# Optimization experiments

Measured on AMD Instinct MI355X. Metric: run time of the kernel, lower is better.

The kernel has to match this reference:

```python
import jax, jax.numpy as jnp
import numpy as np

D_MODEL, D_K, D_V = 1024, 128, 128
B, S = 4, 2048

def setup_inputs() -> dict:
    key = jax.random.key(0)
    k1, k2, k3, k4 = jax.random.split(key, 4)
    return {
        "x_q": jax.random.normal(k1, (B, S, D_MODEL), dtype=jnp.float32),
        "w_q": jax.random.normal(k2, (D_MODEL, D_K), dtype=jnp.float32),
        "w_k": jax.random.normal(k3, (D_MODEL, D_K), dtype=jnp.float32),
        "w_v": jax.random.normal(k4, (D_MODEL, D_V), dtype=jnp.float32),
    }

def reference(x_q, w_q, w_k, w_v):
    # Self-attention: x_k = x_v = x_q (module defaults)
    Q = x_q @ w_q            # [B,S,d_k]
    K = x_q @ w_k            # [B,S,d_k]
    V = x_q @ w_v            # [B,S,d_v]
    scores = jnp.einsum('bqd,bkd->bqk', Q, K) / jnp.sqrt(jnp.float32(D_K))
    # causal mask: tril (row i attends to cols j <= i)
    causal = jnp.tril(jnp.ones((S, S), dtype=bool))
    scores = jnp.where(causal, scores, -jnp.inf)
    # NOTE: softmax over dim=-2 (query axis), per original module
    attention = jax.nn.softmax(scores, axis=-2)
    out = jnp.einsum('bqk,bkv->bqv', attention, V)
    return out, attention
```

## Files before the change

### kernel.cpp

```cpp
#include <hip/hip_runtime.h>
#include <math.h>
#include <stdint.h>

#define B_ 4
#define S_ 2048
#define DM_ 1024
#define DK_ 128

static constexpr float SCALE = 0.08838834764831845f;

typedef __attribute__((ext_vector_type(8))) short short8;
typedef __attribute__((ext_vector_type(4))) float f32x4;
typedef __attribute__((ext_vector_type(4))) unsigned short us4;

__device__ __forceinline__ unsigned short bf16rne(float f){
  unsigned u = __float_as_uint(f);
  unsigned r = (u + 0x7FFFu + ((u>>16)&1u)) >> 16;
  return (unsigned short)r;
}
__device__ __forceinline__ float bf16tof(unsigned short h){
  return __uint_as_float((unsigned)h << 16);
}
__device__ __forceinline__ void gload16(const void* g, void* l){
  __builtin_amdgcn_global_load_lds(
      (const __attribute__((address_space(1))) void*)g,
      (__attribute__((address_space(3))) void*)l, 16, 0, 0);
}

__global__ __launch_bounds__(256) void xconv_kernel(
    const float* __restrict__ X,
    unsigned short* __restrict__ Xth, unsigned short* __restrict__ Xtl)
{
  const int kt = blockIdx.x & 31, mb = blockIdx.x >> 5;
  const int tid = threadIdx.x;
  const int unit = tid & 127, half = tid >> 7;
  const int g = unit >> 5, row = unit & 31;
  const float* src = X + (size_t)(mb*32 + row)*DM_ + kt*32 + g*8;
  float4 a = *reinterpret_cast<const float4*>(src);
  float4 b = *reinterpret_cast<const float4*>(src + 4);
  unsigned short* dst = (half ? Xtl : Xth) + ((size_t)(mb*32 + kt)*128 + unit)*8;
  if(half == 0){
    us4 h0 = {bf16rne(a.x),bf16rne(a.y),bf16rne(a.z),bf16rne(a.w)};
    us4 h1 = {bf16rne(b.x),bf16rne(b.y),bf16rne(b.z),bf16rne(b.w)};
    *(us4*)dst = h0; *(us4*)(dst+4) = h1;
  } else {
    us4 l0 = {bf16rne(a.x - bf16tof(bf16rne(a.x))), bf16rne(a.y - bf16tof(bf16rne(a.y))),
              bf16rne(a.z - bf16tof(bf16rne(a.z))), bf16rne(a.w - bf16tof(bf16rne(a.w)))};
    us4 l1 = {bf16rne(b.x - bf16tof(bf16rne(b.x))), bf16rne(b.y - bf16tof(bf16rne(b.y))),
              bf16rne(b.z - bf16tof(bf16rne(b.z))), bf16rne(b.w - bf16tof(bf16rne(b.w)))};
    *(us4*)dst = l0; *(us4*)(dst+4) = l1;
  }
}

__global__ __launch_bounds__(256) void wconv_kernel(
    const float* __restrict__ Wq, const float* __restrict__ Wk, const float* __restrict__ Wv,
    unsigned short* __restrict__ Wth, unsigned short* __restrict__ Wtl)
{
  const int t = blockIdx.x;
  const int which = blockIdx.y;
  const float* W = (which==0) ? Wq : ((which==1) ? Wk : Wv);
  const int tid = threadIdx.x;
  const size_t obase = ((size_t)which*32 + t)*5120;
  #pragma unroll
  for(int it=0; it<2; ++it){
    int idx = tid + 256*it;
    int col = idx & 127, g = idx >> 7;
    unsigned short hs[8], ls[8];
    #pragma unroll
    for(int j=0;j<8;j++){
      float f = W[(size_t)(t*32 + g*8 + j)*DK_ + col];
      unsigned short h = bf16rne(f);
      hs[j] = h;
      ls[j] = bf16rne(f - bf16tof(h));
    }
    size_t o = obase + (size_t)col*40 + g*8;
    *(us4*)&Wth[o]   = us4{hs[0],hs[1],hs[2],hs[3]};
    *(us4*)&Wth[o+4] = us4{hs[4],hs[5],hs[6],hs[7]};
    *(us4*)&Wtl[o]   = us4{ls[0],ls[1],ls[2],ls[3]};
    *(us4*)&Wtl[o+4] = us4{ls[4],ls[5],ls[6],ls[7]};
  }
}

__global__ __launch_bounds__(256) void qkv_mfma_kernel(
    const unsigned short* __restrict__ Xth, const unsigned short* __restrict__ Xtl,
    const unsigned short* __restrict__ Wth, const unsigned short* __restrict__ Wtl,
    unsigned short* __restrict__ Qh, unsigned short* __restrict__ Ql,
    unsigned short* __restrict__ Kh, unsigned short* __restrict__ Kl,
    unsigned short* __restrict__ Vth)
{
  __shared__ __align__(16) unsigned char smem[49152];
  const int tid = threadIdx.x;
  const int w = tid >> 6, lane = tid & 63;
  const int l15 = lane & 15, g = lane >> 4;
  const int which = blockIdx.y;
  const bool vOnly = (which == 2);
  const int m0 = blockIdx.x * 32;
  const int mb = blockIdx.x;
  const unsigned char* Wh8 = (const unsigned char*)(Wth + (size_t)which*32*5120);
  const unsigned char* Wl8 = (const unsigned char*)(Wtl + (size_t)which*32*5120);
  const unsigned short* Asrc = ((w < 2) ? Xth : Xtl) + (size_t)(mb*32)*1024 + (w & 1)*512 + lane*8;
  const unsigned Adst = (unsigned)((w & 1)*1024) + ((w < 2) ? 0u : 2048u);
  const bool aSkip = (vOnly && w >= 2);

  if(!aSkip) gload16(Asrc, smem + Adst);
  #pragma unroll
  for(int ii=0; ii<5; ++ii){
    int i = w + 4*ii;
    if(vOnly && i >= 10) continue;
    const unsigned char* src = (i<10) ? (Wh8 + i*1024) : (Wl8 + (i-10)*1024);
    unsigned dst = 8192u + ((i<10) ? (unsigned)i*1024u : 10240u + (unsigned)(i-10)*1024u);
    gload16(src + lane*16, smem + dst);
  }

  f32x4 acc[4] = {f32x4{0,0,0,0},f32x4{0,0,0,0},f32x4{0,0,0,0},f32x4{0,0,0,0}};
  const int r = w >> 1, c0 = (w & 1)*4;
  const int aoff = (g*32 + r*16 + l15)*8;
  int buf = 0;
  for(int t=0; t<32; ++t){
    __syncthreads();
    if(t+1 < 32){
      if(!aSkip) gload16(Asrc + (size_t)(t+1)*1024, smem + (buf^1)*4096 + Adst);
      const unsigned char* WhT = Wh8 + (size_t)(t+1)*10240;
      const unsigned char* WlT = Wl8 + (size_t)(t+1)*10240;
      unsigned bbase = 8192u + (unsigned)(buf^1)*20480u;
      #pragma unroll
      for(int ii=0; ii<5; ++ii){
        int i = w + 4*ii;
        if(vOnly && i >= 10) continue;
        const unsigned char* src = (i<10) ? (WhT + i*1024) : (WlT + (i-10)*1024);
        unsigned dst = bbase + ((i<10) ? (unsigned)i*1024u : 10240u + (unsigned)(i-10)*1024u);
        gload16(src + lane*16, smem + dst);
      }
    }
    const unsigned short* Ab = (const unsigned short*)(smem + buf*4096);
    const unsigned short* Bhc = (const unsigned short*)(smem + 8192 + buf*20480);
    const unsigned short* Blc = Bhc + 5120;
    short8 ah = *(const short8*)&Ab[aoff];
    if(vOnly){
      #pragma unroll
      for(int c=0;c<4;c++){
        int boff = ((c0+c)*16 + l15)*40 + g*8;
        short8 bh = *(const short8*)&Bhc[boff];
        acc[c] = __builtin_amdgcn_mfma_f32_16x16x32_bf16(ah, bh, acc[c], 0, 0, 0);
      }
    } else {
      short8 al = *(const short8*)&Ab[1024 + aoff];
      #pragma unroll
      for(int c=0;c<4;c++){
        int boff = ((c0+c)*16 + l15)*40 + g*8;
        short8 bh = *(const short8*)&Bhc[boff];
        short8 bl = *(const short8*)&Blc[boff];
        acc[c] = __builtin_amdgcn_mfma_f32_16x16x32_bf16(ah, bh, acc[c], 0, 0, 0);
        acc[c] = __builtin_amdgcn_mfma_f32_16x16x32_bf16(ah, bl, acc[c], 0, 0, 0);
        acc[c] = __builtin_amdgcn_mfma_f32_16x16x32_bf16(al, bh, acc[c], 0, 0, 0);
      }
    }
    buf ^= 1;
  }
  const int b = m0 >> 11;
  const int orow0 = g*4;
  if(which != 2){
    unsigned short* Oh = (which==0) ? Qh : Kh;
    unsigned short* Ol = (which==0) ? Ql : Kl;
    #pragma unroll
    for(int c=0;c<4;c++){
      int col = (c0+c)*16 + l15;
      #pragma unroll
      for(int j=0;j<4;j++){
        float f = acc[c][j];
        unsigned short h = bf16rne(f);
        unsigned short lo = bf16rne(f - bf16tof(h));
        size_t o = (size_t)(m0 + r*16 + orow0 + j)*DK_ + col;
        Oh[o] = h; Ol[o] = lo;
      }
    }
  } else {
    __syncthreads();
    float* Tmp = (float*)smem;
    #pragma unroll
    for(int c=0;c<4;c++){
      int col = (c0+c)*16 + l15;
      #pragma unroll
      for(int j=0;j<4;j++)
        Tmp[(r*16 + orow0 + j)*133 + col] = acc[c][j];
    }
    __syncthreads();
    const int s0 = m0 & (S_-1);
    #pragma unroll
    for(int l2=0;l2<16;l2++){
      int p = tid + 256*l2;
      int d = p >> 5, rr = p & 31;
      Vth[(size_t)(b*DK_ + d)*S_ + s0 + rr] = bf16rne(Tmp[rr*133 + d]);
    }
  }
}

__global__ __launch_bounds__(256) void scores_kernel(
    const unsigned short* __restrict__ Qh, const unsigned short* __restrict__ Ql,
    const unsigned short* __restrict__ Kh, const unsigned short* __restrict__ Kl,
    float* __restrict__ attn, float* __restrict__ cmaxpart, float* __restrict__ csumpart)
{
  const int tj = blockIdx.x, ti = blockIdx.y, b = blockIdx.z;
  const int tid = threadIdx.x;
  const int q0 = ti*64, k0 = tj*64;
  if(tj > ti){
    float4 z = {0.f,0.f,0.f,0.f};
    #pragma unroll
    for(int l=0;l<4;l++){
      int p = tid + 256*l;
      int r = p >> 4, c = (p & 15) << 2;
      *reinterpret_cast<float4*>(&attn[((size_t)(b*S_) + q0 + r)*S_ + k0 + c]) = z;
    }
    return;
  }
  __shared__ __align__(16) unsigned short sm[16384];
  __shared__ float cred[16][64];
  __shared__ float csum[16][64];
  __shared__ float maxsh[64];
  const int w = tid >> 6, lane = tid & 63, l15 = lane & 15, g = lane >> 4;
  const unsigned short* tsrc[4] = {Qh, Ql, Kh, Kl};
  f32x4 acc[4] = {f32x4{0,0,0,0},f32x4{0,0,0,0},f32x4{0,0,0,0},f32x4{0,0,0,0}};
  for(int kh=0; kh<2; ++kh){
    __syncthreads();
    #pragma unroll
    for(int i=0;i<8;i++){
      int c = w + 4*i;
      int uu = c*64 + lane;
      int tile = uu >> 9;
      int u = uu & 511;
      int row = u >> 3, sl = u & 7;
      int ssl = sl ^ (row & 7);
      int gr = (tile < 2) ? (q0 + row) : (k0 + row);
      gload16(tsrc[tile] + (size_t)(b*S_ + gr)*DK_ + kh*64 + ssl*8,
              (unsigned char*)sm + (unsigned)c*1024u);
    }
    __syncthreads();
    const unsigned short* Qhs = sm;
    const unsigned short* Qls = sm + 4096;
    const unsigned short* Khs = sm + 8192;
    const unsigned short* Kls = sm + 12288;
    #pragma unroll
    for(int ks=0; ks<2; ++ks){
      int arow = w*16 + l15;
      int ao = arow*64 + (((ks*4 + g) ^ (arow & 7)) << 3);
      short8 ah = *(const short8*)&Qhs[ao];
      short8 al = *(const short8*)&Qls[ao];
      #pragma unroll
      for(int c=0;c<4;c++){
        int brow = c*16 + l15;
        int bo = brow*64 + (((ks*4 + g) ^ (brow & 7)) << 3);
        short8 bh = *(const short8*)&Khs[bo];
        short8 bl = *(const short8*)&Kls[bo];
        acc[c] = __builtin_amdgcn_mfma_f32_16x16x32_bf16(ah, bh, acc[c], 0, 0, 0);
        acc[c] = __builtin_amdgcn_mfma_f32_16x16x32_bf16(ah, bl, acc[c], 0, 0, 0);
        acc[c] = __builtin_amdgcn_mfma_f32_16x16x32_bf16(al, bh, acc[c], 0, 0, 0);
      }
    }
  }
  const bool full = (ti > tj);
  const int qbase = q0 + w*16 + g*4;
  #pragma unroll
  for(int c=0;c<4;c++){
    int kcol = k0 + c*16 + l15;
    float cm = -INFINITY;
    #pragma unroll
    for(int j=0;j<4;j++){
      int q = qbase + j;
      float s = acc[c][j]*SCALE;
      bool valid = full || (q >= kcol);
      attn[((size_t)(b*S_) + q)*S_ + kcol] = valid ? s : 0.f;
      if(valid) cm = fmaxf(cm, s);
    }
    cred[w*4 + g][c*16 + l15] = cm;
  }
  __syncthreads();
  if(tid < 64){
    float m = cred[0][tid];
    #pragma unroll
    for(int gg=1;gg<16;gg++) m = fmaxf(m, cred[gg][tid]);
    maxsh[tid] = m;
    cmaxpart[((size_t)(b*S_) + k0 + tid)*32 + ti] = m;
  }
  __syncthreads();
  #pragma unroll
  for(int c=0;c<4;c++){
    int col = c*16 + l15;
    int kcol = k0 + col;
    float mcol = maxsh[col];
    float ps = 0.f;
    #pragma unroll
    for(int j=0;j<4;j++){
      int q = qbase + j;
      bool valid = full || (q >= kcol);
      if(valid) ps += __expf(acc[c][j]*SCALE - mcol);
    }
    csum[w*4 + g][col] = ps;
  }
  __syncthreads();
  if(tid < 64){
    float s = 0.f;
    #pragma unroll
    for(int gg=0;gg<16;gg++) s += csum[gg][tid];
    csumpart[((size_t)(b*S_) + k0 + tid)*32 + ti] = s;
  }
}

__global__ __launch_bounds__(256) void colreduce_kernel(
    const float* __restrict__ cmaxpart, const float* __restrict__ csumpart,
    float* __restrict__ cmaxf, float* __restrict__ rcol)
{
  int i = blockIdx.x*256 + threadIdx.x;
  if(i >= B_*S_) return;
  int k = i & (S_-1);
  int t0 = k >> 6;
  float M = -INFINITY;
  for(int t=t0; t<32; t++) M = fmaxf(M, cmaxpart[(size_t)i*32 + t]);
  float s = 0.f;
  for(int t=t0; t<32; t++) s += csumpart[(size_t)i*32 + t] * __expf(cmaxpart[(size_t)i*32 + t] - M);
  cmaxf[i] = M;
  rcol[i] = 1.0f / s;
}

__global__ __launch_bounds__(256) void pv_kernel(
    float* __restrict__ attn, const float* __restrict__ cmaxf,
    const float* __restrict__ rcol,
    const unsigned short* __restrict__ Vth,
    float* __restrict__ part, int ns)
{
  __shared__ __align__(16) unsigned short sm[17408];
  unsigned short* Ahs = sm;
  unsigned short* Als = sm + 4608;
  unsigned short* VhsL = sm + 9216;
  const int b = blockIdx.z, tid = threadIdx.x;
  const int sp = blockIdx.y;
  const int w = tid >> 6, lane = tid & 63, l15 = lane & 15, g = lane >> 4;
  const int t = 31 - (int)blockIdx.x;
  const int q0 = t*64;
  const int nch = t + 1;
  const int lo = (sp*nch)/ns, hi = ((sp+1)*nch)/ns;
  f32x4 acc[8] = {f32x4{0,0,0,0},f32x4{0,0,0,0},f32x4{0,0,0,0},f32x4{0,0,0,0},
                  f32x4{0,0,0,0},f32x4{0,0,0,0},f32x4{0,0,0,0},f32x4{0,0,0,0}};
  const int er = tid >> 4, ekq = (tid & 15) << 2;
  const unsigned short* Vb = Vth + (size_t)(b*DK_)*S_;
  for(int ch=lo; ch<hi; ++ch){
    const int k0c = ch*64;
    float4 m4 = *reinterpret_cast<const float4*>(&cmaxf[b*S_ + k0c + ekq]);
    float4 r4 = *reinterpret_cast<const float4*>(&rcol[b*S_ + k0c + ekq]);
    const bool diag = (ch == t);
    __syncthreads();
    #pragma unroll
    for(int v=0; v<4; ++v){
      int idx = v*256 + tid;
      int row = idx >> 3, sl = idx & 7;
      int ssl = sl ^ (row & 7);
      gload16(Vb + (size_t)row*S_ + k0c + ssl*8, (unsigned char*)VhsL + idx*16);
    }
    #pragma unroll
    for(int rr=0; rr<4; ++rr){
      int row = rr*16 + er;
      size_t ea = ((size_t)(b*S_) + q0 + row)*S_ + k0c + ekq;
      float4 sv = *reinterpret_cast<const float4*>(&attn[ea]);
      float p0 = __expf(sv.x - m4.x)*r4.x;
      float p1 = __expf(sv.y - m4.y)*r4.y;
      float p2 = __expf(sv.z - m4.z)*r4.z;
      float p3 = __expf(sv.w - m4.w)*r4.w;
      if(diag){
        p0 = (row >= ekq+0) ? p0 : 0.f;
        p1 = (row >= ekq+1) ? p1 : 0.f;
        p2 = (row >= ekq+2) ? p2 : 0.f;
        p3 = (row >= ekq+3) ? p3 : 0.f;
      }
      float4 pv4 = {p0,p1,p2,p3};
      *reinterpret_cast<float4*>(&attn[ea]) = pv4;
      unsigned short h0=bf16rne(p0), h1=bf16rne(p1), h2=bf16rne(p2), h3=bf16rne(p3);
      *(us4*)&Ahs[row*72 + ekq] = us4{h0,h1,h2,h3};
      *(us4*)&Als[row*72 + ekq] = us4{ bf16rne(p0-bf16tof(h0)), bf16rne(p1-bf16tof(h1)),
                                       bf16rne(p2-bf16tof(h2)), bf16rne(p3-bf16tof(h3)) };
    }
    __syncthreads();
    #pragma unroll
    for(int ks=0; ks<2; ++ks){
      int ao = (w*16 + l15)*72 + ks*32 + g*8;
      short8 ah = *(const short8*)&Ahs[ao];
      short8 al = *(const short8*)&Als[ao];
      #pragma unroll
      for(int c=0;c<8;c++){
        int row = c*16 + l15;
        int bo = row*64 + (((ks*4 + g) ^ (l15 & 7)) << 3);
        short8 bh = *(const short8*)&VhsL[bo];
        acc[c] = __builtin_amdgcn_mfma_f32_16x16x32_bf16(ah, bh, acc[c], 0, 0, 0);
        acc[c] = __builtin_amdgcn_mfma_f32_16x16x32_bf16(al, bh, acc[c], 0, 0, 0);
      }
    }
  }
  float* pout = part + (((size_t)(sp*B_ + b))*S_ + q0)*DK_;
  #pragma unroll
  for(int c=0;c<8;c++){
    #pragma unroll
    for(int j=0;j<4;j++){
      int qrow = w*16 + g*4 + j;
      pout[(size_t)qrow*DK_ + c*16 + l15] = acc[c][j];
    }
  }
}

__global__ __launch_bounds__(256) void pvreduce_kernel(
    const float* __restrict__ part, float* __restrict__ out, int ns)
{
  const int N4 = (B_*S_*DK_)/4;
  int i = blockIdx.x*256 + threadIdx.x;
  if(i >= N4) return;
  const float4* p = reinterpret_cast<const float4*>(part);
  float4 a = p[i];
  for(int s=1; s<ns; ++s){
    float4 q = p[(size_t)s*N4 + i];
    a.x += q.x; a.y += q.y; a.z += q.z; a.w += q.w;
  }
  reinterpret_cast<float4*>(out)[i] = a;
}

extern "C" void kernel_launch(void* const* d_in, const int* in_sizes, int n_in,
                              void* d_out, int out_size, void* d_ws, size_t ws_size,
                              hipStream_t stream)
{
  (void)in_sizes; (void)n_in; (void)out_size;
  const float* X  = (const float*)d_in[0];
  const float* Wq = (const float*)d_in[1];
  const float* Wk = (const float*)d_in[2];
  const float* Wv = (const float*)d_in[3];
  float* out  = (float*)d_out;
  float* attn = out + (size_t)B_*S_*DK_;

  unsigned short* Xth = (unsigned short*)attn;
  unsigned short* Xtl = Xth + (size_t)8388608;

  float* ws = (float*)d_ws;
  float* cmaxf    = ws;
  float* rcol     = ws + 8192;
  float* csumpart = ws + 16384;
  float* cmaxpart = ws + 278528;
  unsigned short* Wth = (unsigned short*)(ws + 540672);
  unsigned short* Wtl = (unsigned short*)(ws + 786432);
  unsigned short* Qh  = (unsigned short*)(ws + 1032192);
  unsigned short* Ql  = (unsigned short*)(ws + 1556480);
  unsigned short* Kh  = (unsigned short*)(ws + 2080768);
  unsigned short* Kl  = (unsigned short*)(ws + 2605056);
  unsigned short* Vth = (unsigned short*)(ws + 3129344);
  const size_t base = 3653632;
  float* part    = ws + base;

  int ns = 8;
  if(ws_size < (base + (size_t)8*1048576)*sizeof(float)) ns = 4;
  if(ws_size < (base + (size_t)4*1048576)*sizeof(float)) ns = 2;
  if(ws_size < (base + (size_t)2*1048576)*sizeof(float)) ns = 1;

  xconv_kernel<<<dim3(8192), dim3(256), 0, stream>>>(X, Xth, Xtl);
  wconv_kernel<<<dim3(32,3), dim3(256), 0, stream>>>(Wq, Wk, Wv, Wth, Wtl);
  qkv_mfma_kernel<<<dim3(256,3), dim3(256), 0, stream>>>(Xth, Xtl, Wth, Wtl, Qh, Ql, Kh, Kl, Vth);
  scores_kernel<<<dim3(32,32,4), dim3(256), 0, stream>>>(Qh, Ql, Kh, Kl, attn, cmaxpart, csumpart);
  colreduce_kernel<<<dim3(32), dim3(256), 0, stream>>>(cmaxpart, csumpart, cmaxf, rcol);
  pv_kernel<<<dim3(32,ns,4), dim3(256), 0, stream>>>(attn, cmaxf, rcol, Vth, part, ns);
  pvreduce_kernel<<<dim3(1024), dim3(256), 0, stream>>>(part, out, ns);
}
```

Baseline: 111.9 us.

## Merge conversion kernels, drop low-bf16 P term, skip empty PV splits

Fuses the X and W fp32-to-bf16 split conversion kernels into one launch to save a kernel launch. In the PV kernel, drops the low-order bf16 residual of the attention probabilities, which halves the MFMAs and LDS traffic for the P operand at some accuracy cost. Empty split blocks now return early, and the reduction skips partial buffers that such blocks never wrote.

```diff
diff --git a/kernel.cpp b/kernel.cpp
--- a/kernel.cpp
+++ b/kernel.cpp
@@ -27,57 +27,56 @@
       (__attribute__((address_space(3))) void*)l, 16, 0, 0);
 }
 
-__global__ __launch_bounds__(256) void xconv_kernel(
+__global__ __launch_bounds__(256) void conv_kernel(
     const float* __restrict__ X,
-    unsigned short* __restrict__ Xth, unsigned short* __restrict__ Xtl)
-{
-  const int kt = blockIdx.x & 31, mb = blockIdx.x >> 5;
+    const float* __restrict__ Wq, const float* __restrict__ Wk, const float* __restrict__ Wv,
+    unsigned short* __restrict__ Xth, unsigned short* __restrict__ Xtl,
+    unsigned short* __restrict__ Wth, unsigned short* __restrict__ Wtl)
+{
+  const int bx = blockIdx.x;
   const int tid = threadIdx.x;
-  const int unit = tid & 127, half = tid >> 7;
-  const int g = unit >> 5, row = unit & 31;
-  const float* src = X + (size_t)(mb*32 + row)*DM_ + kt*32 + g*8;
-  float4 a = *reinterpret_cast<const float4*>(src);
-  float4 b = *reinterpret_cast<const float4*>(src + 4);
-  unsigned short* dst = (half ? Xtl : Xth) + ((size_t)(mb*32 + kt)*128 + unit)*8;
-  if(half == 0){
-    us4 h0 = {bf16rne(a.x),bf16rne(a.y),bf16rne(a.z),bf16rne(a.w)};
-    us4 h1 = {bf16rne(b.x),bf16rne(b.y),bf16rne(b.z),bf16rne(b.w)};
-    *(us4*)dst = h0; *(us4*)(dst+4) = h1;
+  if(bx < 8192){
+    const int kt = bx & 31, mb = bx >> 5;
+    const int unit = tid & 127, half = tid >> 7;
+    const int g = unit >> 5, row = unit & 31;
+    const float* src = X + (size_t)(mb*32 + row)*DM_ + kt*32 + g*8;
+    float4 a = *reinterpret_cast<const float4*>(src);
+    float4 b = *reinterpret_cast<const float4*>(src + 4);
+    unsigned short* dst = (half ? Xtl : Xth) + ((size_t)(mb*32 + kt)*128 + unit)*8;
+    if(half == 0){
+      us4 h0 = {bf16rne(a.x),bf16rne(a.y),bf16rne(a.z),bf16rne(a.w)};
+      us4 h1 = {bf16rne(b.x),bf16rne(b.y),bf16rne(b.z),bf16rne(b.w)};
+      *(us4*)dst = h0; *(us4*)(dst+4) = h1;
+    } else {
+      us4 l0 = {bf16rne(a.x - bf16tof(bf16rne(a.x))), bf16rne(a.y - bf16tof(bf16rne(a.y))),
+                bf16rne(a.z - bf16tof(bf16rne(a.z))), bf16rne(a.w - bf16tof(bf16rne(a.w)))};
+      us4 l1 = {bf16rne(b.x - bf16tof(bf16rne(b.x))), bf16rne(b.y - bf16tof(bf16rne(b.y))),
+                bf16rne(b.z - bf16tof(bf16rne(b.z))), bf16rne(b.w - bf16tof(bf16rne(b.w)))};
+      *(us4*)dst = l0; *(us4*)(dst+4) = l1;
+    }
   } else {
-    us4 l0 = {bf16rne(a.x - bf16tof(bf16rne(a.x))), bf16rne(a.y - bf16tof(bf16rne(a.y))),
-              bf16rne(a.z - bf16tof(bf16rne(a.z))), bf16rne(a.w - bf16tof(bf16rne(a.w)))};
-    us4 l1 = {bf16rne(b.x - bf16tof(bf16rne(b.x))), bf16rne(b.y - bf16tof(bf16rne(b.y))),
-              bf16rne(b.z - bf16tof(bf16rne(b.z))), bf16rne(b.w - bf16tof(bf16rne(b.w)))};
-    *(us4*)dst = l0; *(us4*)(dst+4) = l1;
-  }
-}
-
-__global__ __launch_bounds__(256) void wconv_kernel(
-    const float* __restrict__ Wq, const float* __restrict__ Wk, const float* __restrict__ Wv,
-    unsigned short* __restrict__ Wth, unsigned short* __restrict__ Wtl)
-{
-  const int t = blockIdx.x;
-  const int which = blockIdx.y;
-  const float* W = (which==0) ? Wq : ((which==1) ? Wk : Wv);
-  const int tid = threadIdx.x;
-  const size_t obase = ((size_t)which*32 + t)*5120;
-  #pragma unroll
-  for(int it=0; it<2; ++it){
-    int idx = tid + 256*it;
-    int col = idx & 127, g = idx >> 7;
-    unsigned short hs[8], ls[8];
-    #pragma unroll
-    for(int j=0;j<8;j++){
-      float f = W[(size_t)(t*32 + g*8 + j)*DK_ + col];
-      unsigned short h = bf16rne(f);
-      hs[j] = h;
-      ls[j] = bf16rne(f - bf16tof(h));
-    }
-    size_t o = obase + (size_t)col*40 + g*8;
-    *(us4*)&Wth[o]   = us4{hs[0],hs[1],hs[2],hs[3]};
-    *(us4*)&Wth[o+4] = us4{hs[4],hs[5],hs[6],hs[7]};
-    *(us4*)&Wtl[o]   = us4{ls[0],ls[1],ls[2],ls[3]};
-    *(us4*)&Wtl[o+4] = us4{ls[4],ls[5],ls[6],ls[7]};
+    const int wb = bx - 8192;
+    const int which = wb >> 5, t = wb & 31;
+    const float* W = (which==0) ? Wq : ((which==1) ? Wk : Wv);
+    const size_t obase = ((size_t)which*32 + t)*5120;
+    #pragma unroll
+    for(int it=0; it<2; ++it){
+      int idx = tid + 256*it;
+      int col = idx & 127, g = idx >> 7;
+      unsigned short hs[8], ls[8];
+      #pragma unroll
+      for(int j=0;j<8;j++){
+        float f = W[(size_t)(t*32 + g*8 + j)*DK_ + col];
+        unsigned short h = bf16rne(f);
+        hs[j] = h;
+        ls[j] = bf16rne(f - bf16tof(h));
+      }
+      size_t o = obase + (size_t)col*40 + g*8;
+      *(us4*)&Wth[o]   = us4{hs[0],hs[1],hs[2],hs[3]};
+      *(us4*)&Wth[o+4] = us4{hs[4],hs[5],hs[6],hs[7]};
+      *(us4*)&Wtl[o]   = us4{ls[0],ls[1],ls[2],ls[3]};
+      *(us4*)&Wtl[o+4] = us4{ls[4],ls[5],ls[6],ls[7]};
+    }
   }
 }
 
@@ -327,10 +326,9 @@
     const unsigned short* __restrict__ Vth,
     float* __restrict__ part, int ns)
 {
-  __shared__ __align__(16) unsigned short sm[17408];
+  __shared__ __align__(16) unsigned short sm[12800];
   unsigned short* Ahs = sm;
-  unsigned short* Als = sm + 4608;
-  unsigned short* VhsL = sm + 9216;
+  unsigned short* VhsL = sm + 4608;
   const int b = blockIdx.z, tid = threadIdx.x;
   const int sp = blockIdx.y;
   const int w = tid >> 6, lane = tid & 63, l15 = lane & 15, g = lane >> 4;
@@ -338,6 +336,7 @@
   const int q0 = t*64;
   const int nch = t + 1;
   const int lo = (sp*nch)/ns, hi = ((sp+1)*nch)/ns;
+  if(lo >= hi) return;
   f32x4 acc[8] = {f32x4{0,0,0,0},f32x4{0,0,0,0},f32x4{0,0,0,0},f32x4{0,0,0,0},
                   f32x4{0,0,0,0},f32x4{0,0,0,0},f32x4{0,0,0,0},f32x4{0,0,0,0}};
   const int er = tid >> 4, ekq = (tid & 15) << 2;
@@ -372,24 +371,19 @@
       }
       float4 pv4 = {p0,p1,p2,p3};
       *reinterpret_cast<float4*>(&attn[ea]) = pv4;
-      unsigned short h0=bf16rne(p0), h1=bf16rne(p1), h2=bf16rne(p2), h3=bf16rne(p3);
-      *(us4*)&Ahs[row*72 + ekq] = us4{h0,h1,h2,h3};
-      *(us4*)&Als[row*72 + ekq] = us4{ bf16rne(p0-bf16tof(h0)), bf16rne(p1-bf16tof(h1)),
-                                       bf16rne(p2-bf16tof(h2)), bf16rne(p3-bf16tof(h3)) };
+      *(us4*)&Ahs[row*72 + ekq] = us4{bf16rne(p0),bf16rne(p1),bf16rne(p2),bf16rne(p3)};
     }
     __syncthreads();
     #pragma unroll
     for(int ks=0; ks<2; ++ks){
       int ao = (w*16 + l15)*72 + ks*32 + g*8;
       short8 ah = *(const short8*)&Ahs[ao];
-      short8 al = *(const short8*)&Als[ao];
       #pragma unroll
       for(int c=0;c<8;c++){
         int row = c*16 + l15;
         int bo = row*64 + (((ks*4 + g) ^ (l15 & 7)) << 3);
         short8 bh = *(const short8*)&VhsL[bo];
         acc[c] = __builtin_amdgcn_mfma_f32_16x16x32_bf16(ah, bh, acc[c], 0, 0, 0);
-        acc[c] = __builtin_amdgcn_mfma_f32_16x16x32_bf16(al, bh, acc[c], 0, 0, 0);
       }
     }
   }
@@ -405,16 +399,20 @@
 }
 
 __global__ __launch_bounds__(256) void pvreduce_kernel(
-    const float* __restrict__ part, float* __restrict__ out, int ns)
+    const float* __restrict__ part, float* __restrict__ out, int ns, int lns)
 {
   const int N4 = (B_*S_*DK_)/4;
   int i = blockIdx.x*256 + threadIdx.x;
   if(i >= N4) return;
+  int q = (i >> 5) & (S_-1);
+  int nch = (q >> 6) + 1;
   const float4* p = reinterpret_cast<const float4*>(part);
-  float4 a = p[i];
-  for(int s=1; s<ns; ++s){
-    float4 q = p[(size_t)s*N4 + i];
-    a.x += q.x; a.y += q.y; a.z += q.z; a.w += q.w;
+  float4 a = {0.f,0.f,0.f,0.f};
+  for(int s=0; s<ns; ++s){
+    int lo = (s*nch) >> lns, hi = ((s+1)*nch) >> lns;
+    if(lo >= hi) continue;
+    float4 v = p[(size_t)s*N4 + i];
+    a.x += v.x; a.y += v.y; a.z += v.z; a.w += v.w;
   }
   reinterpret_cast<float4*>(out)[i] = a;
 }
@@ -449,16 +447,15 @@
   const size_t base = 3653632;
   float* part    = ws + base;
 
-  int ns = 8;
-  if(ws_size < (base + (size_t)8*1048576)*sizeof(float)) ns = 4;
-  if(ws_size < (base + (size_t)4*1048576)*sizeof(float)) ns = 2;
-  if(ws_size < (base + (size_t)2*1048576)*sizeof(float)) ns = 1;
-
-  xconv_kernel<<<dim3(8192), dim3(256), 0, stream>>>(X, Xth, Xtl);
-  wconv_kernel<<<dim3(32,3), dim3(256), 0, stream>>>(Wq, Wk, Wv, Wth, Wtl);
+  int ns = 8, lns = 3;
+  if(ws_size < (base + (size_t)8*1048576)*sizeof(float)){ ns = 4; lns = 2; }
+  if(ws_size < (base + (size_t)4*1048576)*sizeof(float)){ ns = 2; lns = 1; }
+  if(ws_size < (base + (size_t)2*1048576)*sizeof(float)){ ns = 1; lns = 0; }
+
+  conv_kernel<<<dim3(8288), dim3(256), 0, stream>>>(X, Wq, Wk, Wv, Xth, Xtl, Wth, Wtl);
   qkv_mfma_kernel<<<dim3(256,3), dim3(256), 0, stream>>>(Xth, Xtl, Wth, Wtl, Qh, Ql, Kh, Kl, Vth);
   scores_kernel<<<dim3(32,32,4), dim3(256), 0, stream>>>(Qh, Ql, Kh, Kl, attn, cmaxpart, csumpart);
   colreduce_kernel<<<dim3(32), dim3(256), 0, stream>>>(cmaxpart, csumpart, cmaxf, rcol);
   pv_kernel<<<dim3(32,ns,4), dim3(256), 0, stream>>>(attn, cmaxf, rcol, Vth, part, ns);
-  pvreduce_kernel<<<dim3(1024), dim3(256), 0, stream>>>(part, out, ns);
-}
+  pvreduce_kernel<<<dim3(1024), dim3(256), 0, stream>>>(part, out, ns, lns);
+}
```

New measurement: 104.9 us. -6.3%, faster.
